# Kernel tuning notes

Hardware: AMD Instinct MI355X
Metric: run time of the kernel (lower is better)

Reference implementation:

```python
import jax, jax.numpy as jnp
import numpy as np


def _gelu(x):
    return jax.nn.gelu(x, approximate=False)


def _conv2d(x, w, b, pad=0, dil=1, groups=1):
    y = jax.lax.conv_general_dilated(
        x, w, (1, 1), [(pad, pad), (pad, pad)], rhs_dilation=(dil, dil),
        dimension_numbers=('NCHW', 'OIHW', 'NCHW'), feature_group_count=groups)
    return y + b[None, :, None, None]


def _ln_last(x, g, b, eps=1e-5):
    m = jnp.mean(x, -1, keepdims=True)
    v = jnp.var(x, -1, keepdims=True)
    return (x - m) * jax.lax.rsqrt(v + eps) * g + b


def _ln2d(x, g, b, eps=1e-5):
    # LayerNorm over channel dim of NCHW
    m = jnp.mean(x, 1, keepdims=True)
    v = jnp.var(x, 1, keepdims=True)
    return (x - m) * jax.lax.rsqrt(v + eps) * g[None, :, None, None] + b[None, :, None, None]


def _bilinear(x, py, px):
    # x: [B,C,H,W]; py,px: [B,H,W] float sample coords; zero outside
    B, C, H, W = x.shape
    y0 = jnp.floor(py)
    x0 = jnp.floor(px)
    wy = py - y0
    wx = px - x0
    xf = x.reshape(B, C, H * W)

    def g(yi, xi):
        valid = ((yi >= 0) & (yi < H) & (xi >= 0) & (xi < W)).astype(x.dtype)
        yc = jnp.clip(yi, 0, H - 1).astype(jnp.int32)
        xc = jnp.clip(xi, 0, W - 1).astype(jnp.int32)
        idx = (yc * W + xc).reshape(B, 1, H * W)
        v = jnp.take_along_axis(xf, idx, axis=2).reshape(B, C, H, W)
        return v * valid[:, None]

    return (g(y0, x0) * ((1 - wy) * (1 - wx))[:, None]
            + g(y0, x0 + 1) * ((1 - wy) * wx)[:, None]
            + g(y0 + 1, x0) * (wy * (1 - wx))[:, None]
            + g(y0 + 1, x0 + 1) * (wy * wx)[:, None])


def _deform_dw(x, ow, ob, w, b, dil):
    # modulated deformable depthwise 3x3 conv, offset_groups=1
    B, C, H, W = x.shape
    pad = dil
    off = _conv2d(x, ow, ob, pad=pad, dil=dil)          # [B,27,H,W]
    ox, oy, m = jnp.split(off, 3, axis=1)               # each [B,9,H,W]
    m = jax.nn.sigmoid(m)
    ys = jnp.arange(H, dtype=x.dtype)[None, :, None]
    xs = jnp.arange(W, dtype=x.dtype)[None, None, :]
    acc = jnp.zeros_like(x)
    for ki in range(3):
        for kj in range(3):
            kk = ki * 3 + kj
            py = ys - pad + ki * dil + oy[:, kk]
            px = xs - pad + kj * dil + ox[:, kk]
            s = _bilinear(x, py, px)                    # [B,C,H,W]
            acc = acc + s * m[:, kk][:, None] * w[:, 0, ki, kj][None, :, None, None]
    return acc + b[None, :, None, None]


def _forward(image_embed, inter_prototypes, intra_prototypes, masks,
             proj_w, proj_b, lin_w, lin_b, tok_g, tok_b, alpha,
             in_w, in_b, off0_w, off0_b, dw0_w, dw0_b,
             off1_w, off1_b, dw1_w, dw1_b, cv_w, cv_b, ln_g, ln_b,
             op0_w, op0_b, op1_w, op1_b, op2_w, op2_b,
             out0_w, out0_b, out1_w, out1_b):
    C = image_embed.shape[1]
    scale = C ** -0.5
    # prototype tokens [B,Q,C]
    pt = jnp.einsum('bqc,bnc->bqn', inter_prototypes, intra_prototypes)
    t = jnp.concatenate([inter_prototypes, pt], axis=-1) @ proj_w + proj_b
    t = _gelu(t) @ lin_w + lin_b
    t = _ln_last(t, tok_g, tok_b)
    # mask gating of image features
    pe = jnp.einsum('bnc,bnhw->bchw', intra_prototypes, masks)
    img = image_embed * pe + image_embed
    # DeformAttn
    x = _gelu(_conv2d(img, in_w, in_b))
    a = _deform_dw(x, off0_w, off0_b, dw0_w, dw0_b, dil=1)
    a = _deform_dw(a, off1_w, off1_b, dw1_w, dw1_b, dil=3)
    a = _conv2d(a, cv_w, cv_b)
    x = x * a + img
    x = _ln2d(x, ln_g, ln_b)
    y = _conv2d(x, op0_w, op0_b)
    y = _gelu(_conv2d(y, op1_w, op1_b, pad=1, groups=C))
    y = _conv2d(y, op2_w, op2_b)
    dense = y + x
    # prototype cross-attention over 8 tokens
    attn = jnp.einsum('bchw,bqc->bqhw', dense, t) * scale
    attn = jax.nn.softmax(attn, axis=1)
    attn = jnp.einsum('bqhw,bqc->bchw', attn, t)
    attn = attn + dense * alpha[None, :, None, None]
    o = _gelu(_conv2d(attn, out0_w, out0_b))
    o = _conv2d(o, out1_w, out1_b)
    return o


def setup_inputs():
    key = jax.random.key(0)
    ks = jax.random.split(key, 40)
    B, C, H, W, Q, N = 16, 256, 64, 64, 8, 9
    f32 = jnp.float32

    def rn(k, shp, s=1.0):
        return jax.random.normal(k, shp, f32) * s

    inp = {
        'image_embed': rn(ks[0], (B, C, H, W)),
        'inter_prototypes': rn(ks[1], (B, Q, C)),
        'intra_prototypes': rn(ks[2], (B, N, C)),
        'masks': jax.random.uniform(ks[3], (B, N, H, W), f32),
        'proj_w': rn(ks[4], (C + N, C), 0.02), 'proj_b': jnp.zeros((C,), f32),
        'lin_w': rn(ks[5], (C, C), 0.02), 'lin_b': jnp.zeros((C,), f32),
        'tok_g': 1.0 + rn(ks[6], (C,), 0.05), 'tok_b': rn(ks[7], (C,), 0.05),
        'alpha': jnp.ones((C,), f32) * 0.001,
        'in_w': rn(ks[8], (C, C, 1, 1), 0.02), 'in_b': jnp.zeros((C,), f32),
        'off0_w': rn(ks[9], (27, C, 3, 3), 0.01), 'off0_b': rn(ks[10], (27,), 0.01),
        'dw0_w': rn(ks[11], (C, 1, 3, 3), 0.2), 'dw0_b': jnp.zeros((C,), f32),
        'off1_w': rn(ks[12], (27, C, 3, 3), 0.01), 'off1_b': rn(ks[13], (27,), 0.01),
        'dw1_w': rn(ks[14], (C, 1, 3, 3), 0.2), 'dw1_b': jnp.zeros((C,), f32),
        'cv_w': rn(ks[15], (C, C, 1, 1), 0.02), 'cv_b': jnp.zeros((C,), f32),
        'ln_g': 1.0 + rn(ks[16], (C,), 0.05), 'ln_b': rn(ks[17], (C,), 0.05),
        'op0_w': rn(ks[18], (C, C, 1, 1), 0.02), 'op0_b': jnp.zeros((C,), f32),
        'op1_w': rn(ks[19], (C, 1, 3, 3), 0.2), 'op1_b': jnp.zeros((C,), f32),
        'op2_w': rn(ks[20], (C, C, 1, 1), 0.02), 'op2_b': jnp.zeros((C,), f32),
        'out0_w': rn(ks[21], (C // 2, C, 1, 1), 0.02), 'out0_b': jnp.zeros((C // 2,), f32),
        'out1_w': rn(ks[22], (C, C // 2, 1, 1), 0.02), 'out1_b': jnp.zeros((C,), f32),
    }
    return inp


def reference(image_embed, inter_prototypes, intra_prototypes, masks,
              proj_w, proj_b, lin_w, lin_b, tok_g, tok_b, alpha,
              in_w, in_b, off0_w, off0_b, dw0_w, dw0_b,
              off1_w, off1_b, dw1_w, dw1_b, cv_w, cv_b, ln_g, ln_b,
              op0_w, op0_b, op1_w, op1_b, op2_w, op2_b,
              out0_w, out0_b, out1_w, out1_b):
    return _forward(image_embed, inter_prototypes, intra_prototypes, masks,
                    proj_w, proj_b, lin_w, lin_b, tok_g, tok_b, alpha,
                    in_w, in_b, off0_w, off0_b, dw0_w, dw0_b,
                    off1_w, off1_b, dw1_w, dw1_b, cv_w, cv_b, ln_g, ln_b,
                    op0_w, op0_b, op1_w, op1_b, op2_w, op2_b,
                    out0_w, out0_b, out1_w, out1_b)
```

## Files before the change

### kernel.cpp

```cpp
#include <hip/hip_runtime.h>
#include <math.h>

#define BB 16
#define CC 256
#define HH 64
#define WW 64
#define HWs 4096
#define PP 65536
#define QQ 8
#define NN 9

typedef _Float16 half8_t __attribute__((ext_vector_type(8)));
typedef _Float16 half4_t __attribute__((ext_vector_type(4)));
typedef float floatx4 __attribute__((ext_vector_type(4)));

__device__ __forceinline__ float gelu_f(float x) {
    return 0.5f * x * (1.0f + erff(x * 0.70710678118654752f));
}

__global__ void prep_weights_kernel(const float* __restrict__ off0_w, const float* __restrict__ off1_w,
                                    const float* __restrict__ dw0_w, const float* __restrict__ dw1_w,
                                    const float* __restrict__ op1_w,
                                    const float* __restrict__ in_w, const float* __restrict__ cv_w,
                                    const float* __restrict__ op0_w, const float* __restrict__ op2_w,
                                    const float* __restrict__ out0_w, const float* __restrict__ out1_w,
                                    float* __restrict__ dwt0, float* __restrict__ dwt1,
                                    float* __restrict__ op1t,
                                    _Float16* __restrict__ wh_in, _Float16* __restrict__ wh_cv,
                                    _Float16* __restrict__ wh_op0, _Float16* __restrict__ wh_op2,
                                    _Float16* __restrict__ wh_out0, _Float16* __restrict__ wh_out1,
                                    _Float16* __restrict__ whoff0, _Float16* __restrict__ whoff1) {
    int i = blockIdx.x * 256 + threadIdx.x;
    if (i < 9*256) {
        int c = i & 255;
        int tap = i >> 8;
        dwt0[i] = dw0_w[c*9 + tap];
        dwt1[i] = dw1_w[c*9 + tap];
        op1t[i] = op1_w[c*9 + tap];
    }
    if (i < 65536) {
        wh_in[i]  = (_Float16)in_w[i];
        wh_cv[i]  = (_Float16)cv_w[i];
        wh_op0[i] = (_Float16)op0_w[i];
        wh_op2[i] = (_Float16)op2_w[i];
    }
    if (i < 32768) {
        wh_out0[i] = (_Float16)out0_w[i];
        wh_out1[i] = (_Float16)out1_w[i];
    }
    if (i < 9*32*256) {
        int ci = i & 255;
        int k32 = (i >> 8) & 31;
        int tap = i >> 13;
        float v0 = 0.f, v1 = 0.f;
        if (k32 < 27) {
            v0 = off0_w[(k32*256 + ci)*9 + tap];
            v1 = off1_w[(k32*256 + ci)*9 + tap];
        }
        whoff0[i] = (_Float16)v0;
        whoff1[i] = (_Float16)v1;
    }
}

__global__ void token_kernel(const float* __restrict__ inter, const float* __restrict__ intra,
                             const float* __restrict__ proj_w, const float* __restrict__ proj_b,
                             const float* __restrict__ lin_w, const float* __restrict__ lin_b,
                             const float* __restrict__ tok_g, const float* __restrict__ tok_b,
                             float* __restrict__ t_out) {
    int bq = blockIdx.x;
    int b = bq >> 3, q = bq & 7;
    int c = threadIdx.x;
    __shared__ float inter_s[256];
    __shared__ float pt_s[9];
    __shared__ float g_s[256];
    __shared__ float red[256];
    __shared__ float stat[2];
    inter_s[c] = inter[(b*QQ + q)*CC + c];
    __syncthreads();
    for (int n = 0; n < 9; n++) {
        red[c] = inter_s[c] * intra[(b*NN + n)*CC + c];
        __syncthreads();
        for (int s = 128; s > 0; s >>= 1) {
            if (c < s) red[c] += red[c + s];
            __syncthreads();
        }
        if (c == 0) pt_s[n] = red[0];
        __syncthreads();
    }
    float u = proj_b[c];
    for (int k = 0; k < 256; k++) u += inter_s[k] * proj_w[k*CC + c];
    for (int n = 0; n < 9; n++) u += pt_s[n] * proj_w[(256 + n)*CC + c];
    g_s[c] = gelu_f(u);
    __syncthreads();
    float v = lin_b[c];
    for (int k = 0; k < 256; k++) v += g_s[k] * lin_w[k*CC + c];
    red[c] = v;
    __syncthreads();
    for (int s = 128; s > 0; s >>= 1) { if (c < s) red[c] += red[c + s]; __syncthreads(); }
    if (c == 0) stat[0] = red[0] * (1.0f/256.0f);
    __syncthreads();
    float m = stat[0];
    red[c] = (v - m)*(v - m);
    __syncthreads();
    for (int s = 128; s > 0; s >>= 1) { if (c < s) red[c] += red[c + s]; __syncthreads(); }
    if (c == 0) stat[1] = red[0] * (1.0f/256.0f);
    __syncthreads();
    float var = stat[1];
    float r = rsqrtf(var + 1e-5f);
    t_out[(b*QQ + q)*CC + c] = (v - m) * r * tok_g[c] + tok_b[c];
}

__global__ void img_pe_kernel(const float* __restrict__ ie, const float* __restrict__ intra,
                              const float* __restrict__ masks, float* __restrict__ img) {
    int b = blockIdx.z;
    int c0 = blockIdx.y * 32;
    int s0 = blockIdx.x * 32;
    __shared__ float tile[32][33];
    __shared__ float intra_s[9][32];
    __shared__ float mask_s[9][32];
    int tx = threadIdx.x, ty = threadIdx.y;
    int t = ty*32 + tx;
    for (int i = t; i < 288; i += 256) {
        int n = i >> 5, j = i & 31;
        intra_s[n][j] = intra[(b*NN + n)*CC + c0 + j];
        mask_s[n][j]  = masks[(b*NN + n)*HWs + s0 + j];
    }
    __syncthreads();
    #pragma unroll
    for (int r = 0; r < 4; r++) {
        int cl = ty + 8*r;
        float val = ie[(b*CC + c0 + cl)*HWs + s0 + tx];
        float pe = 0.f;
        #pragma unroll
        for (int n = 0; n < 9; n++) pe += intra_s[n][cl] * mask_s[n][tx];
        tile[cl][tx] = val * (1.0f + pe);
    }
    __syncthreads();
    #pragma unroll
    for (int r = 0; r < 4; r++) {
        int sl = ty + 8*r;
        img[(b*HWs + s0 + sl)*CC + c0 + tx] = tile[tx][sl];
    }
}

template<int CI, int CO, int ACT, int RES, bool INH, int OUT>
__global__ void __launch_bounds__(256) conv1x1_mfma(const void* __restrict__ in, const _Float16* __restrict__ Wh,
        const float* __restrict__ bias, const void* __restrict__ res, float* __restrict__ out,
        _Float16* __restrict__ outh) {
    constexpr int KS = CI/32;
    constexpr int NF = CO/64;
    constexpr int LDR = CI + 8;
    __shared__ __align__(16) _Float16 a_lds[64*LDR];
    int t = threadIdx.x;
    int wid = t >> 6, lane = t & 63;
    int quad = lane >> 4, l16 = lane & 15;
    int p0 = blockIdx.x * 64;
    if (INH) {
        const half8_t* inh = (const half8_t*)in + (size_t)p0*(CI/8);
        for (int i = t; i < 64*(CI/8); i += 256) {
            int r = i/(CI/8), c8 = i%(CI/8);
            *(half8_t*)&a_lds[r*LDR + c8*8] = inh[i];
        }
    } else {
        const float4* inf = (const float4*)in + (size_t)p0*(CI/4);
        for (int i = t; i < 64*(CI/4); i += 256) {
            float4 v = inf[i];
            half4_t hv; hv[0]=(_Float16)v.x; hv[1]=(_Float16)v.y; hv[2]=(_Float16)v.z; hv[3]=(_Float16)v.w;
            int r = i/(CI/4), c4 = i%(CI/4);
            *(half4_t*)&a_lds[r*LDR + c4*4] = hv;
        }
    }
    __syncthreads();
    int n0 = wid*(CO/4);
    floatx4 acc[4][NF];
    #pragma unroll
    for (int mf = 0; mf < 4; mf++)
        #pragma unroll
        for (int nf = 0; nf < NF; nf++)
            #pragma unroll
            for (int r = 0; r < 4; r++) acc[mf][nf][r] = 0.f;
    for (int ks = 0; ks < KS; ks++) {
        int k = ks*32 + quad*8;
        half8_t a[4];
        #pragma unroll
        for (int mf = 0; mf < 4; mf++)
            a[mf] = *(const half8_t*)&a_lds[(mf*16 + l16)*LDR + k];
        half8_t bfr[NF];
        #pragma unroll
        for (int nf = 0; nf < NF; nf++)
            bfr[nf] = *(const half8_t*)&Wh[(size_t)(n0 + nf*16 + l16)*CI + k];
        #pragma unroll
        for (int mf = 0; mf < 4; mf++)
            #pragma unroll
            for (int nf = 0; nf < NF; nf++)
                acc[mf][nf] = __builtin_amdgcn_mfma_f32_16x16x32_f16(a[mf], bfr[nf], acc[mf][nf], 0, 0, 0);
    }
    #pragma unroll
    for (int nf = 0; nf < NF; nf++) {
        int co = n0 + nf*16 + l16;
        float bs = bias[co];
        #pragma unroll
        for (int mf = 0; mf < 4; mf++) {
            #pragma unroll
            for (int r = 0; r < 4; r++) {
                int p = p0 + mf*16 + quad*4 + r;
                float v = acc[mf][nf][r] + bs;
                if (ACT) v = gelu_f(v);
                if (RES == 1) v += ((const float*)res)[(size_t)p*CO + co];
                if (RES == 2) v += (float)((const _Float16*)res)[(size_t)p*CO + co];
                if (OUT == 0 || OUT == 2) out[(size_t)p*CO + co] = v;
                if (OUT == 1 || OUT == 2) outh[(size_t)p*CO + co] = (_Float16)v;
            }
        }
    }
}

template<int DIL>
__global__ void __launch_bounds__(256) off_conv_mfma(const _Float16* __restrict__ x, const _Float16* __restrict__ Wh,
        const float* __restrict__ bias, float* __restrict__ off) {
    constexpr int LDR = 264;
    __shared__ __align__(16) _Float16 xs[70*LDR];
    int raw = blockIdx.x;
    int bh = (raw & 7) * 128 + (raw >> 3);
    int b = bh >> 6, h = bh & 63;
    int t = threadIdx.x;
    int wid = t >> 6, lane = t & 63;
    int quad = lane >> 4, l16 = lane & 15;
    for (int i = t; i < 6*LDR; i += 256) {
        int r = i/LDR, c = i%LDR;
        int row = (r < 3) ? r : (64 + r);
        xs[row*LDR + c] = (_Float16)0.f;
    }
    floatx4 acc[2];
    #pragma unroll
    for (int nf = 0; nf < 2; nf++)
        #pragma unroll
        for (int r = 0; r < 4; r++) acc[nf][r] = 0.f;
    for (int ki = 0; ki < 3; ki++) {
        int hrow = h + (ki - 1)*DIL;
        __syncthreads();
        if (hrow >= 0 && hrow < 64) {
            const half8_t* row = (const half8_t*)(x + ((size_t)(b*64 + hrow)*64) * 256);
            for (int i = t; i < 2048; i += 256) {
                int r = i >> 5, c8 = i & 31;
                *(half8_t*)&xs[(r + 3)*LDR + c8*8] = row[r*32 + c8];
            }
        } else {
            half8_t z = (half8_t)((_Float16)0.f);
            for (int i = t; i < 2048; i += 256) {
                int r = i >> 5, c8 = i & 31;
                *(half8_t*)&xs[(r + 3)*LDR + c8*8] = z;
            }
        }
        __syncthreads();
        #pragma unroll
        for (int kj = 0; kj < 3; kj++) {
            const _Float16* wt = Wh + (size_t)(ki*3 + kj)*32*256;
            int wrow = wid*16 + l16 + (kj - 1)*DIL + 3;
            #pragma unroll
            for (int cs = 0; cs < 8; cs++) {
                int k = cs*32 + quad*8;
                half8_t a = *(const half8_t*)&xs[wrow*LDR + k];
                half8_t b0 = *(const half8_t*)&wt[(size_t)l16*256 + k];
                half8_t b1 = *(const half8_t*)&wt[(size_t)(16 + l16)*256 + k];
                acc[0] = __builtin_amdgcn_mfma_f32_16x16x32_f16(a, b0, acc[0], 0, 0, 0);
                acc[1] = __builtin_amdgcn_mfma_f32_16x16x32_f16(a, b1, acc[1], 0, 0, 0);
            }
        }
    }
    int pbase = (b*64 + h)*64;
    #pragma unroll
    for (int nf = 0; nf < 2; nf++) {
        int kcol = nf*16 + l16;
        if (kcol < 27) {
            float bs = bias[kcol];
            #pragma unroll
            for (int r = 0; r < 4; r++) {
                int w = wid*16 + quad*4 + r;
                off[(size_t)(pbase + w)*27 + kcol] = acc[nf][r] + bs;
            }
        }
    }
}

template<int DIL>
__global__ void __launch_bounds__(256) deform_kernel(const _Float16* __restrict__ src, const float* __restrict__ off,
        const float* __restrict__ dwt, const float* __restrict__ dwb, _Float16* __restrict__ out) {
    int raw = blockIdx.x;
    int swz = (raw & 7) * 256 + (raw >> 3);
    int whalf = swz & 1;
    int bh = swz >> 1;
    int b = bh >> 6, h = bh & 63;
    int t = threadIdx.x;
    int c4 = t & 63;
    int ps = t >> 6;

    __shared__ float4 wq4[288];
    __shared__ int4   iq4[288];

    for (int j = t; j < 288; j += 256) {
        int lw = j / 9;
        int kk = j - lw*9;
        int w = whalf*32 + lw;
        int p = (b*64 + h)*64 + w;
        const float* op = off + (size_t)p*27;
        float ox = op[kk];
        float oy = op[9 + kk];
        float mm = op[18 + kk];
        mm = 1.0f / (1.0f + expf(-mm));
        int ki = kk / 3, kj = kk - ki*3;
        float py = (float)(h - DIL + ki*DIL) + oy;
        float px = (float)(w - DIL + kj*DIL) + ox;
        float y0f = floorf(py), x0f = floorf(px);
        float wy = py - y0f, wx = px - x0f;
        int y0 = (int)y0f, x0 = (int)x0f;
        int y1 = y0 + 1, x1 = x0 + 1;
        float w00 = (1.f - wy)*(1.f - wx)*mm;
        float w01 = (1.f - wy)*wx*mm;
        float w10 = wy*(1.f - wx)*mm;
        float w11 = wy*wx*mm;
        bool yv0 = (y0 >= 0) && (y0 < 64);
        bool yv1 = (y1 >= 0) && (y1 < 64);
        bool xv0 = (x0 >= 0) && (x0 < 64);
        bool xv1 = (x1 >= 0) && (x1 < 64);
        int y0c = min(max(y0, 0), 63), y1c = min(max(y1, 0), 63);
        int x0c = min(max(x0, 0), 63), x1c = min(max(x1, 0), 63);
        int base = b*4096;
        float4 wv;
        wv.x = (yv0 && xv0) ? w00 : 0.f;
        wv.y = (yv0 && xv1) ? w01 : 0.f;
        wv.z = (yv1 && xv0) ? w10 : 0.f;
        wv.w = (yv1 && xv1) ? w11 : 0.f;
        wq4[j] = wv;
        int4 iv;
        iv.x = (base + y0c*64 + x0c) << 9;
        iv.y = (base + y0c*64 + x1c) << 9;
        iv.z = (base + y1c*64 + x0c) << 9;
        iv.w = (base + y1c*64 + x1c) << 9;
        iq4[j] = iv;
    }
    __syncthreads();

    float4 dwv[9];
    #pragma unroll
    for (int kk = 0; kk < 9; kk++) dwv[kk] = ((const float4*)dwt)[kk*64 + c4];
    float4 bv = ((const float4*)dwb)[c4];
    const char* srcb = (const char*)src + (size_t)c4*8;
    for (int i = 0; i < 8; i++) {
        int lw = ps*8 + i;
        int w = whalf*32 + lw;
        int p = (b*64 + h)*64 + w;
        float4 acc = make_float4(0.f,0.f,0.f,0.f);
        #pragma unroll
        for (int kk = 0; kk < 9; kk++) {
            int j = lw*9 + kk;
            float4 wv = wq4[j];
            int4 iv = iq4[j];
            int o0 = __builtin_amdgcn_readfirstlane(iv.x);
            int o1 = __builtin_amdgcn_readfirstlane(iv.y);
            int o2 = __builtin_amdgcn_readfirstlane(iv.z);
            int o3 = __builtin_amdgcn_readfirstlane(iv.w);
            half4_t v0 = *(const half4_t*)(srcb + o0);
            half4_t v1 = *(const half4_t*)(srcb + o1);
            half4_t v2 = *(const half4_t*)(srcb + o2);
            half4_t v3 = *(const half4_t*)(srcb + o3);
            float sx = (float)v0[0]*wv.x + (float)v1[0]*wv.y + (float)v2[0]*wv.z + (float)v3[0]*wv.w;
            float sy = (float)v0[1]*wv.x + (float)v1[1]*wv.y + (float)v2[1]*wv.z + (float)v3[1]*wv.w;
            float sz = (float)v0[2]*wv.x + (float)v1[2]*wv.y + (float)v2[2]*wv.z + (float)v3[2]*wv.w;
            float sw = (float)v0[3]*wv.x + (float)v1[3]*wv.y + (float)v2[3]*wv.z + (float)v3[3]*wv.w;
            acc.x += sx * dwv[kk].x;
            acc.y += sy * dwv[kk].y;
            acc.z += sz * dwv[kk].z;
            acc.w += sw * dwv[kk].w;
        }
        half4_t o4;
        o4[0] = (_Float16)(acc.x + bv.x);
        o4[1] = (_Float16)(acc.y + bv.y);
        o4[2] = (_Float16)(acc.z + bv.z);
        o4[3] = (_Float16)(acc.w + bv.w);
        ((half4_t*)out)[(size_t)p*64 + c4] = o4;
    }
}

__global__ void __launch_bounds__(256) gate_ln_kernel(const _Float16* __restrict__ x, const _Float16* __restrict__ a,
        const float* __restrict__ img, const float* __restrict__ g, const float* __restrict__ bb,
        _Float16* __restrict__ out) {
    int t = threadIdx.x;
    int lane = t & 63;
    int wv = t >> 6;
    int p = blockIdx.x*4 + wv;
    half4_t xh = ((const half4_t*)x)[p*64 + lane];
    half4_t ah = ((const half4_t*)a)[p*64 + lane];
    float4 iv = ((const float4*)img)[p*64 + lane];
    float4 v;
    v.x = (float)xh[0]*(float)ah[0] + iv.x;
    v.y = (float)xh[1]*(float)ah[1] + iv.y;
    v.z = (float)xh[2]*(float)ah[2] + iv.z;
    v.w = (float)xh[3]*(float)ah[3] + iv.w;
    float s = v.x + v.y + v.z + v.w;
    float s2 = v.x*v.x + v.y*v.y + v.z*v.z + v.w*v.w;
    #pragma unroll
    for (int o = 1; o < 64; o <<= 1) { s += __shfl_xor(s, o); s2 += __shfl_xor(s2, o); }
    float m = s * (1.f/256.f);
    float var = s2 * (1.f/256.f) - m*m;
    float r = rsqrtf(var + 1e-5f);
    float4 gv = ((const float4*)g)[lane];
    float4 bv = ((const float4*)bb)[lane];
    half4_t o4;
    o4[0] = (_Float16)((v.x - m)*r*gv.x + bv.x);
    o4[1] = (_Float16)((v.y - m)*r*gv.y + bv.y);
    o4[2] = (_Float16)((v.z - m)*r*gv.z + bv.z);
    o4[3] = (_Float16)((v.w - m)*r*gv.w + bv.w);
    ((half4_t*)out)[p*64 + lane] = o4;
}

__global__ void __launch_bounds__(256) dw3x3_kernel(const _Float16* __restrict__ in, const float* __restrict__ wt,
        const float* __restrict__ bias, _Float16* __restrict__ out) {
    int raw = blockIdx.x;
    int swz = (raw & 7) * 2048 + (raw >> 3);
    int gid = swz*256 + threadIdx.x;
    int c4 = gid & 63;
    int p = gid >> 6;
    int w = p & 63;
    int h = (p >> 6) & 63;
    int b = p >> 12;
    float4 acc = ((const float4*)bias)[c4];
    #pragma unroll
    for (int ki = 0; ki < 3; ki++) {
        int hh = h + ki - 1;
        if (hh < 0 || hh >= 64) continue;
        #pragma unroll
        for (int kj = 0; kj < 3; kj++) {
            int wwp = w + kj - 1;
            if (wwp < 0 || wwp >= 64) continue;
            half4_t v = ((const half4_t*)in)[((b*64 + hh)*64 + wwp)*64 + c4];
            float4 wv = ((const float4*)wt)[(ki*3 + kj)*64 + c4];
            acc.x += (float)v[0]*wv.x; acc.y += (float)v[1]*wv.y;
            acc.z += (float)v[2]*wv.z; acc.w += (float)v[3]*wv.w;
        }
    }
    half4_t o4;
    o4[0] = (_Float16)gelu_f(acc.x);
    o4[1] = (_Float16)gelu_f(acc.y);
    o4[2] = (_Float16)gelu_f(acc.z);
    o4[3] = (_Float16)gelu_f(acc.w);
    ((half4_t*)out)[p*64 + c4] = o4;
}

__global__ void __launch_bounds__(256) attn_kernel(const _Float16* __restrict__ dense, const float* __restrict__ tok,
        const float* __restrict__ alpha, _Float16* __restrict__ out) {
    __shared__ float4 t_s[8*64];
    __shared__ float4 al_s[64];
    int bh = blockIdx.x;
    int b = bh >> 6, h = bh & 63;
    int t = threadIdx.x;
    for (int i = t; i < 512; i += 256) t_s[i] = ((const float4*)tok)[b*512 + i];
    if (t < 64) al_s[t] = ((const float4*)alpha)[t];
    __syncthreads();
    int lane = t & 63, ps = t >> 6;
    for (int i = 0; i < 16; i++) {
        int w = ps*16 + i;
        int p = (b*64 + h)*64 + w;
        half4_t dh = ((const half4_t*)dense)[(size_t)p*64 + lane];
        float4 dv;
        dv.x = (float)dh[0]; dv.y = (float)dh[1]; dv.z = (float)dh[2]; dv.w = (float)dh[3];
        float sc[8];
        #pragma unroll
        for (int q = 0; q < 8; q++) {
            float4 tv = t_s[q*64 + lane];
            float partial = dv.x*tv.x + dv.y*tv.y + dv.z*tv.z + dv.w*tv.w;
            #pragma unroll
            for (int o = 1; o < 64; o <<= 1) partial += __shfl_xor(partial, o);
            sc[q] = partial * 0.0625f;
        }
        float mx = sc[0];
        #pragma unroll
        for (int q = 1; q < 8; q++) mx = fmaxf(mx, sc[q]);
        float e[8]; float denom = 0.f;
        #pragma unroll
        for (int q = 0; q < 8; q++) { e[q] = expf(sc[q] - mx); denom += e[q]; }
        float inv = 1.0f / denom;
        float4 al = al_s[lane];
        float4 o4;
        o4.x = dv.x*al.x; o4.y = dv.y*al.y; o4.z = dv.z*al.z; o4.w = dv.w*al.w;
        #pragma unroll
        for (int q = 0; q < 8; q++) {
            float wq = e[q]*inv;
            float4 tv = t_s[q*64 + lane];
            o4.x += wq*tv.x; o4.y += wq*tv.y; o4.z += wq*tv.z; o4.w += wq*tv.w;
        }
        half4_t oh;
        oh[0] = (_Float16)o4.x; oh[1] = (_Float16)o4.y;
        oh[2] = (_Float16)o4.z; oh[3] = (_Float16)o4.w;
        ((half4_t*)out)[(size_t)p*64 + lane] = oh;
    }
}

__global__ void nhwc_to_nchw_kernel(const float* __restrict__ in, float* __restrict__ out) {
    int b = blockIdx.z;
    int c0 = blockIdx.y*32, s0 = blockIdx.x*32;
    __shared__ float tile[32][33];
    int tx = threadIdx.x, ty = threadIdx.y;
    #pragma unroll
    for (int r = 0; r < 4; r++) {
        int sl = ty + 8*r;
        tile[tx][sl] = in[(b*HWs + s0 + sl)*CC + c0 + tx];
    }
    __syncthreads();
    #pragma unroll
    for (int r = 0; r < 4; r++) {
        int cl = ty + 8*r;
        out[(b*CC + c0 + cl)*HWs + s0 + tx] = tile[cl][tx];
    }
}

extern "C" void kernel_launch(void* const* d_in, const int* in_sizes, int n_in,
                              void* d_out, int out_size, void* d_ws, size_t ws_size,
                              hipStream_t stream) {
    const float* image_embed = (const float*)d_in[0];
    const float* inter_p     = (const float*)d_in[1];
    const float* intra_p     = (const float*)d_in[2];
    const float* masks       = (const float*)d_in[3];
    const float* proj_w      = (const float*)d_in[4];
    const float* proj_b      = (const float*)d_in[5];
    const float* lin_w       = (const float*)d_in[6];
    const float* lin_b       = (const float*)d_in[7];
    const float* tok_g       = (const float*)d_in[8];
    const float* tok_b       = (const float*)d_in[9];
    const float* alpha       = (const float*)d_in[10];
    const float* in_w        = (const float*)d_in[11];
    const float* in_b        = (const float*)d_in[12];
    const float* off0_w      = (const float*)d_in[13];
    const float* off0_b      = (const float*)d_in[14];
    const float* dw0_w       = (const float*)d_in[15];
    const float* dw0_b       = (const float*)d_in[16];
    const float* off1_w      = (const float*)d_in[17];
    const float* off1_b      = (const float*)d_in[18];
    const float* dw1_w       = (const float*)d_in[19];
    const float* dw1_b       = (const float*)d_in[20];
    const float* cv_w        = (const float*)d_in[21];
    const float* cv_b        = (const float*)d_in[22];
    const float* ln_g        = (const float*)d_in[23];
    const float* ln_b        = (const float*)d_in[24];
    const float* op0_w       = (const float*)d_in[25];
    const float* op0_b       = (const float*)d_in[26];
    const float* op1_w       = (const float*)d_in[27];
    const float* op1_b       = (const float*)d_in[28];
    const float* op2_w       = (const float*)d_in[29];
    const float* op2_b       = (const float*)d_in[30];
    const float* out0_w      = (const float*)d_in[31];
    const float* out0_b      = (const float*)d_in[32];
    const float* out1_w      = (const float*)d_in[33];
    const float* out1_b      = (const float*)d_in[34];
    (void)ws_size; (void)in_sizes; (void)n_in; (void)out_size;

    float* ws = (float*)d_ws;
    const size_t BIG = (size_t)PP * CC;
    float* A   = ws;
    float* Bb  = A + BIG;
    float* Cb  = Bb + BIG;
    float* OFF = Cb + BIG;
    float* TOK = OFF + (size_t)PP*27;
    float* DWT0 = TOK + BB*QQ*CC;
    float* DWT1 = DWT0 + 9*256;
    float* OP1T = DWT1 + 9*256;
    _Float16* WH_IN   = (_Float16*)(OP1T + 9*256);
    _Float16* WH_CV   = WH_IN + 65536;
    _Float16* WH_OP0  = WH_CV + 65536;
    _Float16* WH_OP2  = WH_OP0 + 65536;
    _Float16* WH_OUT0 = WH_OP2 + 65536;
    _Float16* WH_OUT1 = WH_OUT0 + 32768;
    _Float16* WHOFF0  = WH_OUT1 + 32768;
    _Float16* WHOFF1  = WHOFF0 + 9*32*256;
    _Float16* XH   = (_Float16*)Bb;
    _Float16* A1H  = XH + (size_t)PP*CC;
    _Float16* A2H  = (_Float16*)Cb;
    _Float16* AH   = A2H + (size_t)PP*CC;
    _Float16* XLNH = (_Float16*)d_out;
    _Float16* Y0H  = (_Float16*)A;
    _Float16* Y1H  = Y0H + (size_t)PP*CC;
    _Float16* DENH = (_Float16*)Cb;
    _Float16* ATH  = (_Float16*)Bb;
    _Float16* O0H  = (_Float16*)Cb + (size_t)PP*CC;

    prep_weights_kernel<<<(9*32*256 + 255)/256, 256, 0, stream>>>(
        off0_w, off1_w, dw0_w, dw1_w, op1_w,
        in_w, cv_w, op0_w, op2_w, out0_w, out1_w,
        DWT0, DWT1, OP1T,
        WH_IN, WH_CV, WH_OP0, WH_OP2, WH_OUT0, WH_OUT1, WHOFF0, WHOFF1);
    token_kernel<<<BB*QQ, 256, 0, stream>>>(inter_p, intra_p, proj_w, proj_b,
                                            lin_w, lin_b, tok_g, tok_b, TOK);
    img_pe_kernel<<<dim3(HWs/32, CC/32, BB), dim3(32,8), 0, stream>>>(image_embed, intra_p, masks, A);
    conv1x1_mfma<256,256,1,0,false,1><<<PP/64, 256, 0, stream>>>(A, WH_IN, in_b, nullptr, nullptr, XH);
    off_conv_mfma<1><<<BB*HH, 256, 0, stream>>>(XH, WHOFF0, off0_b, OFF);
    deform_kernel<1><<<BB*HH*2, 256, 0, stream>>>(XH, OFF, DWT0, dw0_b, A1H);
    off_conv_mfma<3><<<BB*HH, 256, 0, stream>>>(A1H, WHOFF1, off1_b, OFF);
    deform_kernel<3><<<BB*HH*2, 256, 0, stream>>>(A1H, OFF, DWT1, dw1_b, A2H);
    conv1x1_mfma<256,256,0,0,true,1><<<PP/64, 256, 0, stream>>>(A2H, WH_CV, cv_b, nullptr, nullptr, AH);
    gate_ln_kernel<<<PP/4, 256, 0, stream>>>(XH, AH, A, ln_g, ln_b, XLNH);
    conv1x1_mfma<256,256,0,0,true,1><<<PP/64, 256, 0, stream>>>(XLNH, WH_OP0, op0_b, nullptr, nullptr, Y0H);
    dw3x3_kernel<<<PP*64/256, 256, 0, stream>>>(Y0H, OP1T, op1_b, Y1H);
    conv1x1_mfma<256,256,0,2,true,1><<<PP/64, 256, 0, stream>>>(Y1H, WH_OP2, op2_b, XLNH, nullptr, DENH);
    attn_kernel<<<BB*HH, 256, 0, stream>>>(DENH, TOK, alpha, ATH);
    conv1x1_mfma<256,128,1,0,true,1><<<PP/64, 256, 0, stream>>>(ATH, WH_OUT0, out0_b, nullptr, nullptr, O0H);
    conv1x1_mfma<128,256,0,0,true,0><<<PP/64, 256, 0, stream>>>(O0H, WH_OUT1, out1_b, nullptr, A, nullptr);
    nhwc_to_nchw_kernel<<<dim3(HWs/32, CC/32, BB), dim3(32,8), 0, stream>>>(A, (float*)d_out);
}
```

Measured before the change: 914.0 us.

## Use MFMA for token attention, fuse NCHW output transpose, batch deform gathers

The per-pixel token attention is rewritten to use MFMA for both the score and the weighted-sum matmuls, with 64 pixels per block and fp16 tokens staged in LDS. This replaces the wavefront shuffle reductions. The final 1x1 conv gains an output mode that writes NCHW directly, so the separate transpose kernel and its fp32 round trip are removed. The deform kernel now issues all 36 gathers before the arithmetic, keeps the depthwise weights in LDS, and sets a min-blocks launch bound. In exchange, the NCHW stores are strided and register pressure may rise.

Result: faster. 813.4 us (-11.0%).

```diff
diff --git a/kernel.cpp b/kernel.cpp
--- a/kernel.cpp
+++ b/kernel.cpp
@@ -195,6 +195,7 @@
             for (int nf = 0; nf < NF; nf++)
                 acc[mf][nf] = __builtin_amdgcn_mfma_f32_16x16x32_f16(a[mf], bfr[nf], acc[mf][nf], 0, 0, 0);
     }
+    size_t bb = (size_t)(p0 >> 12) * ((size_t)CO * HWs) + (size_t)(p0 & 4095);
     #pragma unroll
     for (int nf = 0; nf < NF; nf++) {
         int co = n0 + nf*16 + l16;
@@ -210,6 +211,7 @@
                 if (RES == 2) v += (float)((const _Float16*)res)[(size_t)p*CO + co];
                 if (OUT == 0 || OUT == 2) out[(size_t)p*CO + co] = v;
                 if (OUT == 1 || OUT == 2) outh[(size_t)p*CO + co] = (_Float16)v;
+                if (OUT == 3) out[bb + (size_t)co*HWs + (mf*16 + quad*4 + r)] = v;
             }
         }
     }
@@ -284,7 +286,7 @@
 }
 
 template<int DIL>
-__global__ void __launch_bounds__(256) deform_kernel(const _Float16* __restrict__ src, const float* __restrict__ off,
+__global__ void __launch_bounds__(256, 3) deform_kernel(const _Float16* __restrict__ src, const float* __restrict__ off,
         const float* __restrict__ dwt, const float* __restrict__ dwb, _Float16* __restrict__ out) {
     int raw = blockIdx.x;
     int swz = (raw & 7) * 256 + (raw >> 3);
@@ -297,6 +299,9 @@
 
     __shared__ float4 wq4[288];
     __shared__ int4   iq4[288];
+    __shared__ float  dw_lds[9*256];
+
+    for (int i = t; i < 9*256; i += 256) dw_lds[i] = dwt[i];
 
     for (int j = t; j < 288; j += 256) {
         int lw = j / 9;
@@ -341,37 +346,39 @@
     }
     __syncthreads();
 
-    float4 dwv[9];
-    #pragma unroll
-    for (int kk = 0; kk < 9; kk++) dwv[kk] = ((const float4*)dwt)[kk*64 + c4];
     float4 bv = ((const float4*)dwb)[c4];
     const char* srcb = (const char*)src + (size_t)c4*8;
     for (int i = 0; i < 8; i++) {
         int lw = ps*8 + i;
+        int jb = lw*9;
         int w = whalf*32 + lw;
         int p = (b*64 + h)*64 + w;
-        float4 acc = make_float4(0.f,0.f,0.f,0.f);
+        half4_t v[9][4];
         #pragma unroll
         for (int kk = 0; kk < 9; kk++) {
-            int j = lw*9 + kk;
-            float4 wv = wq4[j];
-            int4 iv = iq4[j];
+            int4 iv = iq4[jb + kk];
             int o0 = __builtin_amdgcn_readfirstlane(iv.x);
             int o1 = __builtin_amdgcn_readfirstlane(iv.y);
             int o2 = __builtin_amdgcn_readfirstlane(iv.z);
             int o3 = __builtin_amdgcn_readfirstlane(iv.w);
-            half4_t v0 = *(const half4_t*)(srcb + o0);
-            half4_t v1 = *(const half4_t*)(srcb + o1);
-            half4_t v2 = *(const half4_t*)(srcb + o2);
-            half4_t v3 = *(const half4_t*)(srcb + o3);
-            float sx = (float)v0[0]*wv.x + (float)v1[0]*wv.y + (float)v2[0]*wv.z + (float)v3[0]*wv.w;
-            float sy = (float)v0[1]*wv.x + (float)v1[1]*wv.y + (float)v2[1]*wv.z + (float)v3[1]*wv.w;
-            float sz = (float)v0[2]*wv.x + (float)v1[2]*wv.y + (float)v2[2]*wv.z + (float)v3[2]*wv.w;
-            float sw = (float)v0[3]*wv.x + (float)v1[3]*wv.y + (float)v2[3]*wv.z + (float)v3[3]*wv.w;
-            acc.x += sx * dwv[kk].x;
-            acc.y += sy * dwv[kk].y;
-            acc.z += sz * dwv[kk].z;
-            acc.w += sw * dwv[kk].w;
+            v[kk][0] = *(const half4_t*)(srcb + o0);
+            v[kk][1] = *(const half4_t*)(srcb + o1);
+            v[kk][2] = *(const half4_t*)(srcb + o2);
+            v[kk][3] = *(const half4_t*)(srcb + o3);
+        }
+        float4 acc = make_float4(0.f,0.f,0.f,0.f);
+        #pragma unroll
+        for (int kk = 0; kk < 9; kk++) {
+            float4 wv = wq4[jb + kk];
+            float4 dw = ((const float4*)dw_lds)[kk*64 + c4];
+            float sx = (float)v[kk][0][0]*wv.x + (float)v[kk][1][0]*wv.y + (float)v[kk][2][0]*wv.z + (float)v[kk][3][0]*wv.w;
+            float sy = (float)v[kk][0][1]*wv.x + (float)v[kk][1][1]*wv.y + (float)v[kk][2][1]*wv.z + (float)v[kk][3][1]*wv.w;
+            float sz = (float)v[kk][0][2]*wv.x + (float)v[kk][1][2]*wv.y + (float)v[kk][2][2]*wv.z + (float)v[kk][3][2]*wv.w;
+            float sw = (float)v[kk][0][3]*wv.x + (float)v[kk][1][3]*wv.y + (float)v[kk][2][3]*wv.z + (float)v[kk][3][3]*wv.w;
+            acc.x += sx * dw.x;
+            acc.y += sy * dw.y;
+            acc.z += sz * dw.z;
+            acc.w += sw * dw.w;
         }
         half4_t o4;
         o4[0] = (_Float16)(acc.x + bv.x);
@@ -447,70 +454,95 @@
     ((half4_t*)out)[p*64 + c4] = o4;
 }
 
-__global__ void __launch_bounds__(256) attn_kernel(const _Float16* __restrict__ dense, const float* __restrict__ tok,
-        const float* __restrict__ alpha, _Float16* __restrict__ out) {
-    __shared__ float4 t_s[8*64];
-    __shared__ float4 al_s[64];
-    int bh = blockIdx.x;
-    int b = bh >> 6, h = bh & 63;
+__global__ void __launch_bounds__(256) attn_mfma_kernel(const _Float16* __restrict__ dense,
+        const float* __restrict__ tok, const float* __restrict__ alpha, _Float16* __restrict__ out) {
+    __shared__ __align__(16) _Float16 d_lds[64*264];
+    __shared__ __align__(16) _Float16 t_q[16*264];
+    __shared__ __align__(16) _Float16 t_t[258*24];
+    __shared__ __align__(16) _Float16 w_lds[64*40];
+    __shared__ float al_s[256];
     int t = threadIdx.x;
-    for (int i = t; i < 512; i += 256) t_s[i] = ((const float4*)tok)[b*512 + i];
-    if (t < 64) al_s[t] = ((const float4*)alpha)[t];
-    __syncthreads();
-    int lane = t & 63, ps = t >> 6;
-    for (int i = 0; i < 16; i++) {
-        int w = ps*16 + i;
-        int p = (b*64 + h)*64 + w;
-        half4_t dh = ((const half4_t*)dense)[(size_t)p*64 + lane];
-        float4 dv;
-        dv.x = (float)dh[0]; dv.y = (float)dh[1]; dv.z = (float)dh[2]; dv.w = (float)dh[3];
-        float sc[8];
-        #pragma unroll
-        for (int q = 0; q < 8; q++) {
-            float4 tv = t_s[q*64 + lane];
-            float partial = dv.x*tv.x + dv.y*tv.y + dv.z*tv.z + dv.w*tv.w;
-            #pragma unroll
-            for (int o = 1; o < 64; o <<= 1) partial += __shfl_xor(partial, o);
-            sc[q] = partial * 0.0625f;
-        }
-        float mx = sc[0];
-        #pragma unroll
-        for (int q = 1; q < 8; q++) mx = fmaxf(mx, sc[q]);
-        float e[8]; float denom = 0.f;
-        #pragma unroll
-        for (int q = 0; q < 8; q++) { e[q] = expf(sc[q] - mx); denom += e[q]; }
-        float inv = 1.0f / denom;
-        float4 al = al_s[lane];
-        float4 o4;
-        o4.x = dv.x*al.x; o4.y = dv.y*al.y; o4.z = dv.z*al.z; o4.w = dv.w*al.w;
-        #pragma unroll
-        for (int q = 0; q < 8; q++) {
-            float wq = e[q]*inv;
-            float4 tv = t_s[q*64 + lane];
-            o4.x += wq*tv.x; o4.y += wq*tv.y; o4.z += wq*tv.z; o4.w += wq*tv.w;
-        }
-        half4_t oh;
-        oh[0] = (_Float16)o4.x; oh[1] = (_Float16)o4.y;
-        oh[2] = (_Float16)o4.z; oh[3] = (_Float16)o4.w;
-        ((half4_t*)out)[(size_t)p*64 + lane] = oh;
-    }
-}
-
-__global__ void nhwc_to_nchw_kernel(const float* __restrict__ in, float* __restrict__ out) {
-    int b = blockIdx.z;
-    int c0 = blockIdx.y*32, s0 = blockIdx.x*32;
-    __shared__ float tile[32][33];
-    int tx = threadIdx.x, ty = threadIdx.y;
+    int wid = t >> 6, lane = t & 63;
+    int quad = lane >> 4, l16 = lane & 15;
+    int p0 = blockIdx.x * 64;
+    int b = p0 >> 12;
+
+    for (int i = t; i < 16*264; i += 256) t_q[i] = (_Float16)0.f;
+    for (int i = t; i < 258*24; i += 256) t_t[i] = (_Float16)0.f;
+    for (int i = t; i < 64*40;  i += 256) w_lds[i] = (_Float16)0.f;
+    __syncthreads();
+
+    const half8_t* dh = (const half8_t*)dense + (size_t)p0*32;
+    for (int i = t; i < 2048; i += 256) {
+        int r = i >> 5, c8 = i & 31;
+        *(half8_t*)&d_lds[r*264 + c8*8] = dh[i];
+    }
+    for (int i = t; i < 512; i += 256) {
+        int q = i >> 6, j = i & 63;
+        float4 tv = ((const float4*)tok)[(b*8 + q)*64 + j];
+        int c0 = j*4;
+        t_q[q*264 + c0 + 0] = (_Float16)tv.x;
+        t_q[q*264 + c0 + 1] = (_Float16)tv.y;
+        t_q[q*264 + c0 + 2] = (_Float16)tv.z;
+        t_q[q*264 + c0 + 3] = (_Float16)tv.w;
+        t_t[(c0 + 0)*24 + q] = (_Float16)tv.x;
+        t_t[(c0 + 1)*24 + q] = (_Float16)tv.y;
+        t_t[(c0 + 2)*24 + q] = (_Float16)tv.z;
+        t_t[(c0 + 3)*24 + q] = (_Float16)tv.w;
+    }
+    al_s[t] = alpha[t];
+    __syncthreads();
+
+    floatx4 s4;
+    s4[0]=0.f; s4[1]=0.f; s4[2]=0.f; s4[3]=0.f;
+    #pragma unroll
+    for (int ks = 0; ks < 8; ks++) {
+        int k = ks*32 + quad*8;
+        half8_t a = *(const half8_t*)&d_lds[(wid*16 + l16)*264 + k];
+        half8_t bf = *(const half8_t*)&t_q[l16*264 + k];
+        s4 = __builtin_amdgcn_mfma_f32_16x16x32_f16(a, bf, s4, 0, 0, 0);
+    }
+    float wgt[4];
     #pragma unroll
     for (int r = 0; r < 4; r++) {
-        int sl = ty + 8*r;
-        tile[tx][sl] = in[(b*HWs + s0 + sl)*CC + c0 + tx];
-    }
-    __syncthreads();
-    #pragma unroll
-    for (int r = 0; r < 4; r++) {
-        int cl = ty + 8*r;
-        out[(b*CC + c0 + cl)*HWs + s0 + tx] = tile[cl][tx];
+        float sc = s4[r] * 0.0625f;
+        float mx = sc;
+        mx = fmaxf(mx, __shfl_xor(mx, 1));
+        mx = fmaxf(mx, __shfl_xor(mx, 2));
+        mx = fmaxf(mx, __shfl_xor(mx, 4));
+        float e = expf(sc - mx);
+        float dn = e;
+        dn += __shfl_xor(dn, 1);
+        dn += __shfl_xor(dn, 2);
+        dn += __shfl_xor(dn, 4);
+        wgt[r] = e / dn;
+    }
+    if (l16 < 8) {
+        #pragma unroll
+        for (int r = 0; r < 4; r++)
+            w_lds[(wid*16 + quad*4 + r)*40 + l16] = (_Float16)wgt[r];
+    }
+    __syncthreads();
+
+    half8_t aw = *(const half8_t*)&w_lds[(wid*16 + l16)*40 + quad*8];
+    floatx4 z4; z4[0]=0.f; z4[1]=0.f; z4[2]=0.f; z4[3]=0.f;
+    floatx4 acc[16];
+    #pragma unroll
+    for (int nf = 0; nf < 16; nf++) {
+        half8_t bf = *(const half8_t*)&t_t[(nf*16 + l16)*24 + quad*8];
+        acc[nf] = __builtin_amdgcn_mfma_f32_16x16x32_f16(aw, bf, z4, 0, 0, 0);
+    }
+    #pragma unroll
+    for (int nf = 0; nf < 16; nf++) {
+        int co = nf*16 + l16;
+        float al = al_s[co];
+        #pragma unroll
+        for (int r = 0; r < 4; r++) {
+            int px = wid*16 + quad*4 + r;
+            float d = (float)d_lds[px*264 + co];
+            float o = acc[nf][r] + d*al;
+            out[(size_t)(p0 + px)*256 + co] = (_Float16)o;
+        }
     }
 }
 
@@ -601,8 +633,7 @@
     conv1x1_mfma<256,256,0,0,true,1><<<PP/64, 256, 0, stream>>>(XLNH, WH_OP0, op0_b, nullptr, nullptr, Y0H);
     dw3x3_kernel<<<PP*64/256, 256, 0, stream>>>(Y0H, OP1T, op1_b, Y1H);
     conv1x1_mfma<256,256,0,2,true,1><<<PP/64, 256, 0, stream>>>(Y1H, WH_OP2, op2_b, XLNH, nullptr, DENH);
-    attn_kernel<<<BB*HH, 256, 0, stream>>>(DENH, TOK, alpha, ATH);
+    attn_mfma_kernel<<<PP/64, 256, 0, stream>>>(DENH, TOK, alpha, ATH);
     conv1x1_mfma<256,128,1,0,true,1><<<PP/64, 256, 0, stream>>>(ATH, WH_OUT0, out0_b, nullptr, nullptr, O0H);
-    conv1x1_mfma<128,256,0,0,true,0><<<PP/64, 256, 0, stream>>>(O0H, WH_OUT1, out1_b, nullptr, A, nullptr);
-    nhwc_to_nchw_kernel<<<dim3(HWs/32, CC/32, BB), dim3(32,8), 0, stream>>>(A, (float*)d_out);
-}
+    conv1x1_mfma<128,256,0,0,true,3><<<PP/64, 256, 0, stream>>>(O0H, WH_OUT1, out1_b, nullptr, (float*)d_out, nullptr);
+}
```
